# Performance work log

Measured on AMD Instinct MI355X. Metric: run time of the kernel, lower is better.

## Reference

```python
import jax, jax.numpy as jnp
import numpy as np

R = 131072   # rays
S = 128      # existing samples per ray (existing_bins has S+1 edges)
N_NEW = 64   # new importance samples per ray
HIST_PAD = 1e-5   # NeuSSampler builds PDFSampler(histogram_padding=1e-5)
EPS = 1e-5


def setup_inputs() -> dict:
    key = jax.random.key(0)
    k1, k2, k3, k4 = jax.random.split(key, 4)
    weights = jax.random.uniform(k1, (R, S, 1), dtype=jnp.float32)
    # existing spacing bins must be sorted in [0,1] along the sample axis
    existing_bins = jnp.sort(jax.random.uniform(k2, (R, S + 1), dtype=jnp.float32), axis=-1)
    nears = 0.05 + 0.5 * jax.random.uniform(k3, (R, 1), dtype=jnp.float32)
    fars = nears + 1.0 + 3.0 * jax.random.uniform(k4, (R, 1), dtype=jnp.float32)
    return {"weights": weights, "existing_bins": existing_bins,
            "nears": nears, "fars": fars, "num_samples": N_NEW}


def reference(weights, existing_bins, nears, fars, num_samples):
    # PDFSampler.generate_ray_samples core (eval mode, include_original=False)
    num_bins = num_samples + 1
    w = weights[..., 0] + HIST_PAD                      # [R, S]
    w_sum = jnp.sum(w, axis=-1, keepdims=True)          # [R, 1]
    padding = jax.nn.relu(EPS - w_sum)
    w = w + padding / w.shape[-1]
    w_sum = w_sum + padding
    pdf = w / w_sum                                     # [R, S]
    cdf = jnp.minimum(jnp.ones_like(pdf), jnp.cumsum(pdf, axis=-1))
    cdf = jnp.concatenate([jnp.zeros_like(cdf[..., :1]), cdf], axis=-1)  # [R, S+1]

    # deterministic mid-bin query points (non-stratified branch)
    u = jnp.linspace(0.0, 1.0 - 1.0 / num_bins, num_bins, dtype=cdf.dtype)
    u = u + 1.0 / (2 * num_bins)
    u = jnp.broadcast_to(u, (*cdf.shape[:-1], num_bins))  # [R, num_bins]

    # inverse-CDF: per-ray binary search + gather + linear interp
    inds = jax.vmap(lambda c, q: jnp.searchsorted(c, q, side='right'))(cdf, u)
    last = existing_bins.shape[-1] - 1
    below = jnp.clip(inds - 1, 0, last)
    above = jnp.clip(inds, 0, last)
    cdf_g0 = jnp.take_along_axis(cdf, below, axis=-1)
    bins_g0 = jnp.take_along_axis(existing_bins, below, axis=-1)
    cdf_g1 = jnp.take_along_axis(cdf, above, axis=-1)
    bins_g1 = jnp.take_along_axis(existing_bins, above, axis=-1)
    t = jnp.clip(jnp.nan_to_num((u - cdf_g0) / (cdf_g1 - cdf_g0), nan=0.0,
                                posinf=0.0, neginf=0.0), 0.0, 1.0)
    bins = bins_g0 + t * (bins_g1 - bins_g0)            # [R, num_bins]
    bins = jax.lax.stop_gradient(bins)                  # torch: bins.detach()

    # spacing_to_euclidean_fn for UniformSampler: x*s_far + (1-x)*s_near
    euclidean_bins = bins * fars + (1.0 - bins) * nears  # [R, num_bins]
    return euclidean_bins
```

## Files before the change

kernel.cpp:

```cpp
#include <hip/hip_runtime.h>


__global__ __launch_bounds__(256) void neus_sampler_kernel(
    const float* __restrict__ weights,
    const float* __restrict__ bins_g,
    const float* __restrict__ nears,
    const float* __restrict__ fars,
    float* __restrict__ out,
    int R)
{
    constexpr int S  = 128;
    constexpr int SE = 129;
    constexpr int NB = 65;
    constexpr float HPAD = 1e-5f;

    __shared__ float s_cdf[4][SE + 1];
    __shared__ float s_bin[4][SE + 1];

    const int lane = threadIdx.x & 63;
    const int wv   = threadIdx.x >> 6;
    const int ray  = blockIdx.x * 4 + wv;
    const bool valid = ray < R;
    const int cray = valid ? ray : (R - 1);

    const float2 wpair =
        reinterpret_cast<const float2*>(weights + (size_t)cray * S)[lane];
    const float w0 = wpair.x + HPAD;
    const float w1 = wpair.y + HPAD;

    const float* brow = bins_g + (size_t)cray * SE;
    s_bin[wv][2 * lane]     = brow[2 * lane];
    s_bin[wv][2 * lane + 1] = brow[2 * lane + 1];
    if (lane == 0) s_bin[wv][S] = brow[S];

    float ps = w0 + w1;
    #pragma unroll
    for (int off = 1; off < 64; off <<= 1) {
        float n = __shfl_up(ps, off, 64);
        if (lane >= off) ps += n;
    }
    const float total   = __shfl(ps, 63, 64);
    const float padding = fmaxf(1e-5f - total, 0.0f);
    const float padc    = padding * (1.0f / S);
    const float inv     = 1.0f / (total + padding);

    s_cdf[wv][2 * lane + 1] =
        fminf(1.0f, (ps - w1 + (float)(2 * lane + 1) * padc) * inv);
    s_cdf[wv][2 * lane + 2] =
        fminf(1.0f, (ps + (float)(2 * lane + 2) * padc) * inv);
    if (lane == 0) s_cdf[wv][0] = 0.0f;

    __syncthreads();

    const float nearv = nears[cray];
    const float farv  = fars[cray];
    const float* cdf = s_cdf[wv];
    const float* bnr = s_bin[wv];
    float* orow = out + (size_t)ray * NB;

    auto sample = [&](int j) -> float {
        const float u = (float)(2 * j + 1) * (1.0f / (2.0f * NB));
        int lo = 0, hi = SE;
        while (lo < hi) {
            const int mid = (lo + hi) >> 1;
            if (cdf[mid] <= u) lo = mid + 1; else hi = mid;
        }
        int above = lo;     if (above > S) above = S;
        int below = lo - 1; if (below < 0) below = 0;
        const float c0 = cdf[below], c1 = cdf[above];
        const float b0 = bnr[below], b1 = bnr[above];
        const float denom = c1 - c0;
        const float t = (denom > 0.0f)
            ? fminf(fmaxf((u - c0) / denom, 0.0f), 1.0f) : 0.0f;
        const float b = fmaf(t, b1 - b0, b0);
        return b * farv + (1.0f - b) * nearv;
    };

    const float r_own  = sample(lane);
    const float r_last = sample(64);

    if (valid) {
        orow[lane] = r_own;
        if (lane == 0) orow[NB - 1] = r_last;
    }
}

extern "C" void kernel_launch(void* const* d_in, const int* in_sizes, int n_in,
                              void* d_out, int out_size, void* d_ws, size_t ws_size,
                              hipStream_t stream) {
    const float* weights = (const float*)d_in[0];
    const float* ebins   = (const float*)d_in[1];
    const float* nears   = (const float*)d_in[2];
    const float* fars    = (const float*)d_in[3];
    float* out = (float*)d_out;
    const int R = in_sizes[0] / 128;
    const int blocks = (R + 3) / 4;
    hipLaunchKernelGGL(neus_sampler_kernel, dim3(blocks), dim3(256), 0, stream,
                       weights, ebins, nears, fars, out, R);
}
```

Before: 183.8 us.

## Replace per-sample binary search with per-interval scatter of inverse-CDF samples

Each lane now holds two CDF intervals in registers and works out which of the uniformly spaced query points fall inside them. It then interpolates and writes those outputs directly, instead of every lane binary-searching a shared-memory CDF. Neighbouring CDF and bin values come from wave shuffles, so the shared-memory staging and the block barrier go away. The cost is divergent variable-length loops per lane and scattered stores. The index computation with ceilf at interval edges may disagree with searchsorted at exact boundaries.

```diff
diff --git a/kernel.cpp b/kernel.cpp
--- a/kernel.cpp
+++ b/kernel.cpp
@@ -10,30 +10,22 @@
     int R)
 {
     constexpr int S  = 128;
-    constexpr int SE = 129;
     constexpr int NB = 65;
     constexpr float HPAD = 1e-5f;
 
-    __shared__ float s_cdf[4][SE + 1];
-    __shared__ float s_bin[4][SE + 1];
-
     const int lane = threadIdx.x & 63;
-    const int wv   = threadIdx.x >> 6;
-    const int ray  = blockIdx.x * 4 + wv;
-    const bool valid = ray < R;
-    const int cray = valid ? ray : (R - 1);
+    const int ray  = blockIdx.x * 4 + (threadIdx.x >> 6);
+    if (ray >= R) return;
 
     const float2 wpair =
-        reinterpret_cast<const float2*>(weights + (size_t)cray * S)[lane];
-    const float w0 = wpair.x + HPAD;
+        reinterpret_cast<const float2*>(weights + (size_t)ray * S)[lane];
+    const float* brow = bins_g + (size_t)ray * (S + 1);
+    const float2 bpair = reinterpret_cast<const float2*>(brow)[lane];
+    const float b_last = brow[S];
+
     const float w1 = wpair.y + HPAD;
+    float ps = (wpair.x + HPAD) + w1;
 
-    const float* brow = bins_g + (size_t)cray * SE;
-    s_bin[wv][2 * lane]     = brow[2 * lane];
-    s_bin[wv][2 * lane + 1] = brow[2 * lane + 1];
-    if (lane == 0) s_bin[wv][S] = brow[S];
-
-    float ps = w0 + w1;
     #pragma unroll
     for (int off = 1; off < 64; off <<= 1) {
         float n = __shfl_up(ps, off, 64);
@@ -44,44 +36,47 @@
     const float padc    = padding * (1.0f / S);
     const float inv     = 1.0f / (total + padding);
 
-    s_cdf[wv][2 * lane + 1] =
-        fminf(1.0f, (ps - w1 + (float)(2 * lane + 1) * padc) * inv);
-    s_cdf[wv][2 * lane + 2] =
-        fminf(1.0f, (ps + (float)(2 * lane + 2) * padc) * inv);
-    if (lane == 0) s_cdf[wv][0] = 0.0f;
+    const float c_hi  = fminf(1.0f, fmaf((float)(2 * lane + 2), padc, ps) * inv);
+    const float c_mid = fminf(1.0f, fmaf((float)(2 * lane + 1), padc, ps - w1) * inv);
+    float c_lo = __shfl_up(c_hi, 1, 64);
+    if (lane == 0) c_lo = 0.0f;
 
-    __syncthreads();
+    float b2 = __shfl_down(bpair.x, 1, 64);
+    if (lane == 63) b2 = b_last;
 
-    const float nearv = nears[cray];
-    const float farv  = fars[cray];
-    const float* cdf = s_cdf[wv];
-    const float* bnr = s_bin[wv];
+    const float nearv = nears[ray];
+    const float farv  = fars[ray];
+    const float fmn   = farv - nearv;
     float* orow = out + (size_t)ray * NB;
 
-    auto sample = [&](int j) -> float {
-        const float u = (float)(2 * j + 1) * (1.0f / (2.0f * NB));
-        int lo = 0, hi = SE;
-        while (lo < hi) {
-            const int mid = (lo + hi) >> 1;
-            if (cdf[mid] <= u) lo = mid + 1; else hi = mid;
-        }
-        int above = lo;     if (above > S) above = S;
-        int below = lo - 1; if (below < 0) below = 0;
-        const float c0 = cdf[below], c1 = cdf[above];
-        const float b0 = bnr[below], b1 = bnr[above];
-        const float denom = c1 - c0;
-        const float t = (denom > 0.0f)
-            ? fminf(fmaxf((u - c0) / denom, 0.0f), 1.0f) : 0.0f;
-        const float b = fmaf(t, b1 - b0, b0);
-        return b * farv + (1.0f - b) * nearv;
+    auto jf = [](float c) -> int {
+        int j = (int)ceilf(fmaf(65.0f, c, -0.5f));
+        return j < 0 ? 0 : (j > NB ? NB : j);
     };
 
-    const float r_own  = sample(lane);
-    const float r_last = sample(64);
+    const int j0 = jf(c_lo);
+    const int j1 = jf(c_mid);
+    const int j2 = (lane == 63) ? NB : jf(c_hi);
 
-    if (valid) {
-        orow[lane] = r_own;
-        if (lane == 0) orow[NB - 1] = r_last;
+    {
+        const float d = c_mid - c_lo;
+        for (int j = j0; j < j1; ++j) {
+            const float u = (float)(2 * j + 1) * (1.0f / 130.0f);
+            float t = (d > 0.0f) ? (u - c_lo) / d : 0.0f;
+            t = fminf(fmaxf(t, 0.0f), 1.0f);
+            const float b = fmaf(t, bpair.y - bpair.x, bpair.x);
+            orow[j] = fmaf(b, fmn, nearv);
+        }
+    }
+    {
+        const float d = c_hi - c_mid;
+        for (int j = j1; j < j2; ++j) {
+            const float u = (float)(2 * j + 1) * (1.0f / 130.0f);
+            float t = (d > 0.0f) ? (u - c_mid) / d : 0.0f;
+            t = fminf(fmaxf(t, 0.0f), 1.0f);
+            const float b = fmaf(t, b2 - bpair.y, bpair.y);
+            orow[j] = fmaf(b, fmn, nearv);
+        }
     }
 }
 
```

Result: faster. 171.8 us (-6.5%).
